# Kernel tuning notes

Hardware: AMD Instinct MI355X
Metric: run time of the kernel (lower is better)

Reference implementation:

```python
import jax, jax.numpy as jnp
import numpy as np

B, IN_DIM, LATENT_DIM, EMBED_DIM = 262144, 512, 128, 10000


def setup_inputs() -> dict:
    key = jax.random.key(0)
    k_x, k_y, k_wlv, k_blv, k_wmu, k_bmu, k_we, k_be = jax.random.split(key, 8)
    s_in = 1.0 / np.sqrt(IN_DIM)
    s_e = 1.0 / np.sqrt(EMBED_DIM)
    return {
        "x": jax.random.normal(k_x, (B, IN_DIM), dtype=jnp.float32),
        "y": jax.random.randint(k_y, (B,), 0, EMBED_DIM, dtype=jnp.int32),
        # torch nn.Linear weights are [out_features, in_features]
        "W_logvar": jax.random.uniform(k_wlv, (LATENT_DIM, IN_DIM), minval=-s_in, maxval=s_in, dtype=jnp.float32),
        "b_logvar": jax.random.uniform(k_blv, (LATENT_DIM,), minval=-s_in, maxval=s_in, dtype=jnp.float32),
        "W_mean": jax.random.uniform(k_wmu, (LATENT_DIM, IN_DIM), minval=-s_in, maxval=s_in, dtype=jnp.float32),
        "b_mean": jax.random.uniform(k_bmu, (LATENT_DIM,), minval=-s_in, maxval=s_in, dtype=jnp.float32),
        "W_embed": jax.random.uniform(k_we, (LATENT_DIM, EMBED_DIM), minval=-s_e, maxval=s_e, dtype=jnp.float32),
        "b_embed": jax.random.uniform(k_be, (LATENT_DIM,), minval=-s_e, maxval=s_e, dtype=jnp.float32),
    }


def reference(x, y, W_logvar, b_logvar, W_mean, b_mean, W_embed, b_embed):
    # logvar / mean heads: plain dense GEMMs, x @ W.T + b
    logvar = jnp.einsum("bi,li->bl", x, W_logvar) + b_logvar
    mean = jnp.einsum("bi,li->bl", x, W_mean) + b_mean
    # one_hot(y) @ W_embed.T + b_embed  ==  gather columns of W_embed at y
    embed = jnp.take(W_embed, y, axis=1).T + b_embed  # [B, latent_dim]
    return (logvar, mean, embed)
```

## Files before the change

kernel.cpp:

```cpp
#include <hip/hip_runtime.h>
#include <hip/hip_bf16.h>

#define NB 262144
#define KD 512
#define ED 10000

typedef __attribute__((ext_vector_type(8))) short s8v;
typedef __attribute__((ext_vector_type(4))) float f4v;

typedef __attribute__((address_space(1))) const unsigned int gu32_t;
typedef __attribute__((address_space(3))) unsigned int lu32_t;

__device__ __forceinline__ short f2bf(float f) {
  union { __hip_bfloat16 h; short s; } u;
  u.h = __float2bfloat16(f);
  return u.s;
}

__global__ void prep_w(const float* __restrict__ Wlv, const float* __restrict__ Wmu,
                       unsigned short* __restrict__ wbf) {
  int i = blockIdx.x * 256 + threadIdx.x;
  int row = i >> 9, col = i & 511;
  float v = (row < 128) ? Wlv[(row << 9) | col] : Wmu[((row - 128) << 9) | col];
  union { __hip_bfloat16 h; unsigned short s; } u;
  u.h = __float2bfloat16(v);
  wbf[i] = u.s;
}

__global__ void prep_embT(const float* __restrict__ We, const float* __restrict__ be,
                          float* __restrict__ embT) {
  __shared__ float t[32][129];
  const int v0 = blockIdx.x << 5;
#pragma unroll
  for (int j = 0; j < 16; ++j) {
    int idx = j * 256 + threadIdx.x;
    int l = idx >> 5, vi = idx & 31;
    int v = v0 + vi;
    t[vi][l] = (v < ED) ? We[(size_t)l * ED + v] : 0.f;
  }
  __syncthreads();
#pragma unroll
  for (int j = 0; j < 16; ++j) {
    int idx = j * 256 + threadIdx.x;
    int v = idx >> 7, l = idx & 127;
    if (v0 + v < ED)
      embT[(size_t)(v0 + v) * 128 + l] = t[v][l] + be[l];
  }
}

__global__ __launch_bounds__(512, 4) void gemm_heads(
    const float* __restrict__ x, const unsigned short* __restrict__ wbf,
    const float* __restrict__ blv, const float* __restrict__ bmu,
    float* __restrict__ out) {
  __shared__ char lds[65536];
  const int tid  = threadIdx.x;
  const int lane = tid & 63;
  const int wid  = tid >> 6;
  const int gm   = blockIdx.x << 7;
  const int wm   = wid >> 2;
  const int wn   = wid & 3;
  const float* xblk = x + ((size_t)gm << 9);

  unsigned aSrc[2], aDst[2], bSrc[2], bDst[2];
#pragma unroll
  for (int s = 0; s < 2; ++s) {
    int c = tid + (s << 9);
    { int row = c >> 3, q = c & 7;
      int qp = q ^ ((row & 3) << 1);
      aSrc[s] = (unsigned)(row << 9) + (unsigned)(qp << 2);
      aDst[s] = (unsigned)(c << 4); }
    { int row = c >> 2, q = c & 3;
      int qp = q ^ ((row >> 1) & 3);
      bSrc[s] = (unsigned)(row << 9) + (unsigned)(qp << 3);
      bDst[s] = 32768u + (unsigned)(c << 4); }
  }

  unsigned offA[4], offB[4];
#pragma unroll
  for (int t4 = 0; t4 < 4; ++t4) {
    { int row = (wm << 6) + (t4 << 4) + (lane & 15);
      int q = ((lane >> 4) << 1) ^ ((row & 3) << 1);
      offA[t4] = (unsigned)(row << 7) + (unsigned)(q << 4); }
    { int row = (wn << 6) + (t4 << 4) + (lane & 15);
      int q = (lane >> 4) ^ ((row >> 1) & 3);
      offB[t4] = 32768u + (unsigned)(row << 6) + (unsigned)(q << 4); }
  }

  f4v acc[4][4];
#pragma unroll
  for (int i = 0; i < 4; ++i)
#pragma unroll
    for (int j = 0; j < 4; ++j) acc[i][j] = (f4v)0.f;

#pragma unroll
  for (int s = 0; s < 2; ++s) {
    __builtin_amdgcn_global_load_lds((const gu32_t*)(xblk + aSrc[s]),
                                     (lu32_t*)(lds + aDst[s]), 16, 0, 0);
    __builtin_amdgcn_global_load_lds((const gu32_t*)(wbf + bSrc[s]),
                                     (lu32_t*)(lds + bDst[s]), 16, 0, 0);
  }
  __syncthreads();

  for (int t = 0; t < 16; ++t) {
    const unsigned db = (unsigned)((t & 1) << 14);
    if (t < 15) {
      const int ke = (t + 1) << 5;
      const unsigned db2 = (unsigned)(((t + 1) & 1) << 14);
#pragma unroll
      for (int s = 0; s < 2; ++s) {
        __builtin_amdgcn_global_load_lds((const gu32_t*)(xblk + aSrc[s] + ke),
                                         (lu32_t*)(lds + aDst[s] + db2), 16, 0, 0);
        __builtin_amdgcn_global_load_lds((const gu32_t*)(wbf + bSrc[s] + ke),
                                         (lu32_t*)(lds + bDst[s] + db2), 16, 0, 0);
      }
    }
    s8v bfr[4];
#pragma unroll
    for (int nt = 0; nt < 4; ++nt)
      bfr[nt] = *(const s8v*)(lds + offB[nt] + db);
#pragma unroll
    for (int mt = 0; mt < 4; ++mt) {
      const char* pa = lds + offA[mt] + db;
      float4 a0 = *(const float4*)(pa);
      float4 a1 = *(const float4*)(pa + 16);
      s8v af;
      af[0] = f2bf(a0.x); af[1] = f2bf(a0.y); af[2] = f2bf(a0.z); af[3] = f2bf(a0.w);
      af[4] = f2bf(a1.x); af[5] = f2bf(a1.y); af[6] = f2bf(a1.z); af[7] = f2bf(a1.w);
#pragma unroll
      for (int nt = 0; nt < 4; ++nt)
        acc[mt][nt] = __builtin_amdgcn_mfma_f32_16x16x32_bf16(af, bfr[nt], acc[mt][nt], 0, 0, 0);
    }
    __syncthreads();
  }

  const int col16 = lane & 15;
  const int rsub  = (lane >> 4) << 2;
#pragma unroll
  for (int nt = 0; nt < 4; ++nt) {
    int col = (wn << 6) + (nt << 4) + col16;
    float bias = (col < 128) ? blv[col] : bmu[col - 128];
    float* ob = (col < 128) ? (out + col)
                            : (out + ((size_t)NB << 7) + (col - 128));
#pragma unroll
    for (int mt = 0; mt < 4; ++mt) {
      int row0 = gm + (wm << 6) + (mt << 4) + rsub;
#pragma unroll
      for (int r = 0; r < 4; ++r)
        ob[(size_t)(row0 + r) << 7] = acc[mt][nt][r] + bias;
    }
  }
}

__global__ void embed_fast(const int* __restrict__ y, const float* __restrict__ embT,
                           float* __restrict__ out3) {
  unsigned t = blockIdx.x * 256 + threadIdx.x;
  int b  = t >> 5;
  int l4 = (t & 31) << 2;
  int v  = y[b];
  float4 s = *(const float4*)(embT + (size_t)v * 128 + l4);
  *(float4*)(out3 + ((size_t)b << 7) + l4) = s;
}

__global__ void gemm_naive(const float* __restrict__ x,
                           const float* __restrict__ Wlv, const float* __restrict__ blv,
                           const float* __restrict__ Wmu, const float* __restrict__ bmu,
                           float* __restrict__ out) {
  __shared__ float xr[512];
  int b = blockIdx.x;
  for (int i = threadIdx.x; i < 512; i += 256) xr[i] = x[(size_t)b * 512 + i];
  __syncthreads();
  int c = threadIdx.x;
  const float* w = (c < 128) ? (Wlv + c * 512) : (Wmu + (c - 128) * 512);
  float s = 0.f;
  for (int k = 0; k < 512; ++k) s += xr[k] * w[k];
  s += (c < 128) ? blv[c] : bmu[c - 128];
  float* o = (c < 128) ? (out + (size_t)b * 128 + c)
                       : (out + ((size_t)NB << 7) + (size_t)b * 128 + (c - 128));
  *o = s;
}

__global__ void embed_direct(const int* __restrict__ y, const float* __restrict__ We,
                             const float* __restrict__ be, float* __restrict__ out3) {
  size_t t = (size_t)blockIdx.x * 256 + threadIdx.x;
  int b = (int)(t >> 7), l = (int)(t & 127);
  out3[t] = We[(size_t)l * ED + y[b]] + be[l];
}

extern "C" void kernel_launch(void* const* d_in, const int* in_sizes, int n_in,
                              void* d_out, int out_size, void* d_ws, size_t ws_size,
                              hipStream_t stream) {
  const float* x   = (const float*)d_in[0];
  const int*   y   = (const int*)d_in[1];
  const float* Wlv = (const float*)d_in[2];
  const float* blv = (const float*)d_in[3];
  const float* Wmu = (const float*)d_in[4];
  const float* bmu = (const float*)d_in[5];
  const float* We  = (const float*)d_in[6];
  const float* be  = (const float*)d_in[7];
  float* out  = (float*)d_out;
  float* out3 = out + ((size_t)NB << 8);

  const size_t needW = 256 * 512 * sizeof(unsigned short);
  const size_t needE = needW + (size_t)ED * 128 * sizeof(float);
  unsigned short* wbf = (unsigned short*)d_ws;
  float* embT = (float*)((char*)d_ws + needW);

  if (ws_size >= needW) {
    prep_w<<<512, 256, 0, stream>>>(Wlv, Wmu, wbf);
    gemm_heads<<<NB / 128, 512, 0, stream>>>(x, wbf, blv, bmu, out);
  } else {
    gemm_naive<<<NB, 256, 0, stream>>>(x, Wlv, blv, Wmu, bmu, out);
  }

  if (ws_size >= needE) {
    prep_embT<<<(ED + 31) / 32, 256, 0, stream>>>(We, be, embT);
    embed_fast<<<NB * 32 / 256, 256, 0, stream>>>(y, embT, out3);
  } else {
    embed_direct<<<NB * 128 / 256, 256, 0, stream>>>(y, We, be, out3);
  }
}
```

Before: 315.0 us.

## Fuse prep kernels and embed gather into LDS-free direct-load GEMM

```diff
diff --git a/kernel.cpp b/kernel.cpp
--- a/kernel.cpp
+++ b/kernel.cpp
@@ -8,157 +8,123 @@
 typedef __attribute__((ext_vector_type(8))) short s8v;
 typedef __attribute__((ext_vector_type(4))) float f4v;
 
-typedef __attribute__((address_space(1))) const unsigned int gu32_t;
-typedef __attribute__((address_space(3))) unsigned int lu32_t;
-
 __device__ __forceinline__ short f2bf(float f) {
   union { __hip_bfloat16 h; short s; } u;
   u.h = __float2bfloat16(f);
   return u.s;
 }
 
-__global__ void prep_w(const float* __restrict__ Wlv, const float* __restrict__ Wmu,
-                       unsigned short* __restrict__ wbf) {
-  int i = blockIdx.x * 256 + threadIdx.x;
-  int row = i >> 9, col = i & 511;
-  float v = (row < 128) ? Wlv[(row << 9) | col] : Wmu[((row - 128) << 9) | col];
-  union { __hip_bfloat16 h; unsigned short s; } u;
-  u.h = __float2bfloat16(v);
-  wbf[i] = u.s;
-}
-
-__global__ void prep_embT(const float* __restrict__ We, const float* __restrict__ be,
-                          float* __restrict__ embT) {
+__global__ void prep_all(const float* __restrict__ Wlv, const float* __restrict__ Wmu,
+                         unsigned short* __restrict__ wbf,
+                         const float* __restrict__ We, const float* __restrict__ be,
+                         float* __restrict__ embT) {
   __shared__ float t[32][129];
-  const int v0 = blockIdx.x << 5;
+  if (blockIdx.x < 512) {
+    int i = blockIdx.x * 256 + threadIdx.x;
+    int row = i >> 9, col = i & 511;
+    float v = (row < 128) ? Wlv[(row << 9) | col] : Wmu[((row - 128) << 9) | col];
+    union { __hip_bfloat16 h; unsigned short s; } u;
+    u.h = __float2bfloat16(v);
+    wbf[i] = u.s;
+  } else {
+    const int v0 = (blockIdx.x - 512) << 5;
 #pragma unroll
-  for (int j = 0; j < 16; ++j) {
-    int idx = j * 256 + threadIdx.x;
-    int l = idx >> 5, vi = idx & 31;
-    int v = v0 + vi;
-    t[vi][l] = (v < ED) ? We[(size_t)l * ED + v] : 0.f;
-  }
-  __syncthreads();
+    for (int j = 0; j < 16; ++j) {
+      int idx = j * 256 + threadIdx.x;
+      int l = idx >> 5, vi = idx & 31;
+      int v = v0 + vi;
+      t[vi][l] = (v < ED) ? We[(size_t)l * ED + v] : 0.f;
+    }
+    __syncthreads();
 #pragma unroll
-  for (int j = 0; j < 16; ++j) {
-    int idx = j * 256 + threadIdx.x;
-    int v = idx >> 7, l = idx & 127;
-    if (v0 + v < ED)
-      embT[(size_t)(v0 + v) * 128 + l] = t[v][l] + be[l];
+    for (int j = 0; j < 16; ++j) {
+      int idx = j * 256 + threadIdx.x;
+      int v = idx >> 7, l = idx & 127;
+      if (v0 + v < ED)
+        embT[(size_t)(v0 + v) * 128 + l] = t[v][l] + be[l];
+    }
   }
 }
 
-__global__ __launch_bounds__(512, 4) void gemm_heads(
+__global__ __launch_bounds__(512, 2) void gemm_heads(
     const float* __restrict__ x, const unsigned short* __restrict__ wbf,
     const float* __restrict__ blv, const float* __restrict__ bmu,
-    float* __restrict__ out) {
-  __shared__ char lds[65536];
+    const int* __restrict__ y, const float* __restrict__ embT,
+    float* __restrict__ out, int doEmbed) {
   const int tid  = threadIdx.x;
   const int lane = tid & 63;
   const int wid  = tid >> 6;
+  const int wm   = wid >> 1;
+  const int wn   = wid & 1;
   const int gm   = blockIdx.x << 7;
-  const int wm   = wid >> 2;
-  const int wn   = wid & 3;
-  const float* xblk = x + ((size_t)gm << 9);
+  const int lr   = lane & 15;
+  const int kg   = lane >> 4;
 
-  unsigned aSrc[2], aDst[2], bSrc[2], bDst[2];
+  const float* pa0 = x + (((size_t)(gm + (wm << 5) + lr)) << 9) + (kg << 3);
+  const float* pa1 = pa0 + (16 << 9);
+  const unsigned short* pb[8];
 #pragma unroll
-  for (int s = 0; s < 2; ++s) {
-    int c = tid + (s << 9);
-    { int row = c >> 3, q = c & 7;
-      int qp = q ^ ((row & 3) << 1);
-      aSrc[s] = (unsigned)(row << 9) + (unsigned)(qp << 2);
-      aDst[s] = (unsigned)(c << 4); }
-    { int row = c >> 2, q = c & 3;
-      int qp = q ^ ((row >> 1) & 3);
-      bSrc[s] = (unsigned)(row << 9) + (unsigned)(qp << 3);
-      bDst[s] = 32768u + (unsigned)(c << 4); }
+  for (int nt = 0; nt < 8; ++nt)
+    pb[nt] = wbf + (((size_t)((wn << 7) + (nt << 4) + lr)) << 9) + (kg << 3);
+
+  f4v acc[2][8];
+#pragma unroll
+  for (int m = 0; m < 2; ++m)
+#pragma unroll
+    for (int nt = 0; nt < 8; ++nt) acc[m][nt] = (f4v)0.f;
+
+  for (int t4 = 0; t4 < 4; ++t4) {
+#pragma unroll
+    for (int u = 0; u < 4; ++u) {
+      const int ko = u << 5;
+      float4 a0lo = *(const float4*)(pa0 + ko);
+      float4 a0hi = *(const float4*)(pa0 + ko + 4);
+      float4 a1lo = *(const float4*)(pa1 + ko);
+      float4 a1hi = *(const float4*)(pa1 + ko + 4);
+      s8v af0, af1;
+      af0[0] = f2bf(a0lo.x); af0[1] = f2bf(a0lo.y); af0[2] = f2bf(a0lo.z); af0[3] = f2bf(a0lo.w);
+      af0[4] = f2bf(a0hi.x); af0[5] = f2bf(a0hi.y); af0[6] = f2bf(a0hi.z); af0[7] = f2bf(a0hi.w);
+      af1[0] = f2bf(a1lo.x); af1[1] = f2bf(a1lo.y); af1[2] = f2bf(a1lo.z); af1[3] = f2bf(a1lo.w);
+      af1[4] = f2bf(a1hi.x); af1[5] = f2bf(a1hi.y); af1[6] = f2bf(a1hi.z); af1[7] = f2bf(a1hi.w);
+#pragma unroll
+      for (int nt = 0; nt < 8; ++nt) {
+        s8v bf = *(const s8v*)(pb[nt] + ko);
+        acc[0][nt] = __builtin_amdgcn_mfma_f32_16x16x32_bf16(af0, bf, acc[0][nt], 0, 0, 0);
+        acc[1][nt] = __builtin_amdgcn_mfma_f32_16x16x32_bf16(af1, bf, acc[1][nt], 0, 0, 0);
+      }
+    }
+    pa0 += 128; pa1 += 128;
+#pragma unroll
+    for (int nt = 0; nt < 8; ++nt) pb[nt] += 128;
   }
 
-  unsigned offA[4], offB[4];
+  const int rsub = kg << 2;
 #pragma unroll
-  for (int t4 = 0; t4 < 4; ++t4) {
-    { int row = (wm << 6) + (t4 << 4) + (lane & 15);
-      int q = ((lane >> 4) << 1) ^ ((row & 3) << 1);
-      offA[t4] = (unsigned)(row << 7) + (unsigned)(q << 4); }
-    { int row = (wn << 6) + (t4 << 4) + (lane & 15);
-      int q = (lane >> 4) ^ ((row >> 1) & 3);
-      offB[t4] = 32768u + (unsigned)(row << 6) + (unsigned)(q << 4); }
-  }
-
-  f4v acc[4][4];
-#pragma unroll
-  for (int i = 0; i < 4; ++i)
-#pragma unroll
-    for (int j = 0; j < 4; ++j) acc[i][j] = (f4v)0.f;
-
-#pragma unroll
-  for (int s = 0; s < 2; ++s) {
-    __builtin_amdgcn_global_load_lds((const gu32_t*)(xblk + aSrc[s]),
-                                     (lu32_t*)(lds + aDst[s]), 16, 0, 0);
-    __builtin_amdgcn_global_load_lds((const gu32_t*)(wbf + bSrc[s]),
-                                     (lu32_t*)(lds + bDst[s]), 16, 0, 0);
-  }
-  __syncthreads();
-
-  for (int t = 0; t < 16; ++t) {
-    const unsigned db = (unsigned)((t & 1) << 14);
-    if (t < 15) {
-      const int ke = (t + 1) << 5;
-      const unsigned db2 = (unsigned)(((t + 1) & 1) << 14);
-#pragma unroll
-      for (int s = 0; s < 2; ++s) {
-        __builtin_amdgcn_global_load_lds((const gu32_t*)(xblk + aSrc[s] + ke),
-                                         (lu32_t*)(lds + aDst[s] + db2), 16, 0, 0);
-        __builtin_amdgcn_global_load_lds((const gu32_t*)(wbf + bSrc[s] + ke),
-                                         (lu32_t*)(lds + bDst[s] + db2), 16, 0, 0);
-      }
-    }
-    s8v bfr[4];
-#pragma unroll
-    for (int nt = 0; nt < 4; ++nt)
-      bfr[nt] = *(const s8v*)(lds + offB[nt] + db);
-#pragma unroll
-    for (int mt = 0; mt < 4; ++mt) {
-      const char* pa = lds + offA[mt] + db;
-      float4 a0 = *(const float4*)(pa);
-      float4 a1 = *(const float4*)(pa + 16);
-      s8v af;
-      af[0] = f2bf(a0.x); af[1] = f2bf(a0.y); af[2] = f2bf(a0.z); af[3] = f2bf(a0.w);
-      af[4] = f2bf(a1.x); af[5] = f2bf(a1.y); af[6] = f2bf(a1.z); af[7] = f2bf(a1.w);
-#pragma unroll
-      for (int nt = 0; nt < 4; ++nt)
-        acc[mt][nt] = __builtin_amdgcn_mfma_f32_16x16x32_bf16(af, bfr[nt], acc[mt][nt], 0, 0, 0);
-    }
-    __syncthreads();
-  }
-
-  const int col16 = lane & 15;
-  const int rsub  = (lane >> 4) << 2;
-#pragma unroll
-  for (int nt = 0; nt < 4; ++nt) {
-    int col = (wn << 6) + (nt << 4) + col16;
+  for (int nt = 0; nt < 8; ++nt) {
+    int col = (wn << 7) + (nt << 4) + lr;
     float bias = (col < 128) ? blv[col] : bmu[col - 128];
     float* ob = (col < 128) ? (out + col)
                             : (out + ((size_t)NB << 7) + (col - 128));
 #pragma unroll
-    for (int mt = 0; mt < 4; ++mt) {
-      int row0 = gm + (wm << 6) + (mt << 4) + rsub;
+    for (int m = 0; m < 2; ++m) {
+      int row0 = gm + (wm << 5) + (m << 4) + rsub;
 #pragma unroll
       for (int r = 0; r < 4; ++r)
-        ob[(size_t)(row0 + r) << 7] = acc[mt][nt][r] + bias;
+        ob[(size_t)(row0 + r) << 7] = acc[m][nt][r] + bias;
     }
   }
-}
 
-__global__ void embed_fast(const int* __restrict__ y, const float* __restrict__ embT,
-                           float* __restrict__ out3) {
-  unsigned t = blockIdx.x * 256 + threadIdx.x;
-  int b  = t >> 5;
-  int l4 = (t & 31) << 2;
-  int v  = y[b];
-  float4 s = *(const float4*)(embT + (size_t)v * 128 + l4);
-  *(float4*)(out3 + ((size_t)b << 7) + l4) = s;
+  if (doEmbed) {
+    float* out3 = out + ((size_t)NB << 8);
+    int r  = tid >> 2;
+    int c0 = (tid & 3) << 5;
+    int row = gm + r;
+    int v = y[row];
+    const float4* src = (const float4*)(embT + (size_t)v * 128 + c0);
+    float4* dst = (float4*)(out3 + ((size_t)row << 7) + c0);
+#pragma unroll
+    for (int j = 0; j < 8; ++j) dst[j] = src[j];
+  }
 }
 
 __global__ void gemm_naive(const float* __restrict__ x,
@@ -205,17 +171,15 @@
   unsigned short* wbf = (unsigned short*)d_ws;
   float* embT = (float*)((char*)d_ws + needW);
 
-  if (ws_size >= needW) {
-    prep_w<<<512, 256, 0, stream>>>(Wlv, Wmu, wbf);
-    gemm_heads<<<NB / 128, 512, 0, stream>>>(x, wbf, blv, bmu, out);
+  if (ws_size >= needE) {
+    prep_all<<<512 + 313, 256, 0, stream>>>(Wlv, Wmu, wbf, We, be, embT);
+    gemm_heads<<<NB / 128, 512, 0, stream>>>(x, wbf, blv, bmu, y, embT, out, 1);
+  } else if (ws_size >= needW) {
+    prep_all<<<512, 256, 0, stream>>>(Wlv, Wmu, wbf, We, be, (float*)d_ws);
+    gemm_heads<<<NB / 128, 512, 0, stream>>>(x, wbf, blv, bmu, y, nullptr, out, 0);
+    embed_direct<<<NB * 128 / 256, 256, 0, stream>>>(y, We, be, out3);
   } else {
     gemm_naive<<<NB, 256, 0, stream>>>(x, Wlv, blv, Wmu, bmu, out);
-  }
-
-  if (ws_size >= needE) {
-    prep_embT<<<(ED + 31) / 32, 256, 0, stream>>>(We, be, embT);
-    embed_fast<<<NB * 32 / 256, 256, 0, stream>>>(y, embT, out3);
-  } else {
     embed_direct<<<NB * 128 / 256, 256, 0, stream>>>(y, We, be, out3);
   }
 }
```

Measured after the change: 513.9 us. +63.2%, slower.
